# Optimization experiments

Measured on AMD Instinct MI355X. Metric: run time of the kernel, lower is better.

The kernel has to match this reference:

```python
import jax, jax.numpy as jnp
import numpy as np

N_JOINTS = 24

def _rodrigues(r):
    # r: [B, J, 3] axis-angle -> [B, J, 3, 3] rotation matrices
    theta = jnp.clip(jnp.linalg.norm(r, axis=-1, keepdims=True), 1e-6)  # [B,J,1]
    rh = r / theta
    z = jnp.zeros_like(rh[..., :1])
    # skew-symmetric matrix m
    m = jnp.stack([
        jnp.concatenate([z, -rh[..., 2:3], rh[..., 1:2]], -1),
        jnp.concatenate([rh[..., 2:3], z, -rh[..., 0:1]], -1),
        jnp.concatenate([-rh[..., 1:2], rh[..., 0:1], z], -1),
    ], axis=-2)  # [B,J,3,3]
    rrT = rh[..., :, None] * rh[..., None, :]  # outer product [B,J,3,3]
    cos = jnp.cos(theta)[..., None]
    sin = jnp.sin(theta)[..., None]
    eye = jnp.eye(3, dtype=r.dtype)
    return cos * eye + (1.0 - cos) * rrT + sin * m

def _with_zeros(Rm, t):
    # Rm: [B,3,3], t: [B,3] -> [B,4,4] homogeneous transform
    B = Rm.shape[0]
    top = jnp.concatenate([Rm, t[:, :, None]], axis=-1)  # [B,3,4]
    bot = jnp.broadcast_to(jnp.array([0.0, 0.0, 0.0, 1.0], Rm.dtype), (B, 1, 4))
    return jnp.concatenate([top, bot], axis=1)

def _keypoints(v, idx):
    # v: [B,N,3], idx: [G,K] vertex-index groups -> [B,G,3] via (max+min)/2
    g = v[:, idx]  # [B,G,K,3] irregular gather
    return (g.max(axis=2) + g.min(axis=2)) * 0.5

def setup_inputs() -> dict:
    key = jax.random.key(0)
    ks = jax.random.split(key, 8)
    B, N, P, K = 64, 40000, 100, 128
    beta = jax.random.normal(ks[0], (B, P), jnp.float32)
    pose = jax.random.normal(ks[1], (B, N_JOINTS * 3), jnp.float32) * 0.3
    trans = jax.random.normal(ks[2], (B, 3), jnp.float32)
    shapedirs = jax.random.normal(ks[3], (P, 3 * N), jnp.float32) * 0.01
    v_template = jax.random.normal(ks[4], (N, 3), jnp.float32)
    w = jax.random.uniform(ks[5], (N, N_JOINTS), jnp.float32)
    weights = w / w.sum(axis=1, keepdims=True)  # LBS weights sum to 1
    reorder_index = jnp.arange(N_JOINTS, dtype=jnp.int64 if jax.config.jax_enable_x64 else jnp.int32)
    # kinematic tree: parent[i] < i (binary-tree shape stands in for the rabbit skeleton)
    parent = jnp.concatenate([jnp.zeros(1, jnp.int32), (jnp.arange(1, N_JOINTS, dtype=jnp.int32) - 1) // 2])
    joint_idx = jax.random.randint(ks[6], (N_JOINTS - 1, K), 0, N)
    add_idx = jax.random.randint(ks[7], (7, K), 0, N)
    return {"beta": beta, "pose": pose, "trans": trans, "shapedirs": shapedirs,
            "v_template": v_template, "weights": weights, "reorder_index": reorder_index,
            "parent": parent, "joint_idx": joint_idx, "add_idx": add_idx}

def reference(beta, pose, trans, shapedirs, v_template, weights,
              reorder_index, parent, joint_idx, add_idx):
    B = beta.shape[0]
    pose = pose.reshape(B, N_JOINTS, 3)[:, reorder_index]
    # blend shapes: v_shaped = beta @ shapedirs + template
    v_posed = (beta @ shapedirs + v_template.reshape(-1)).reshape(B, -1, 3)  # [B,N,3]
    # joints from vertex-group (max+min)/2, root is zero
    J = jnp.concatenate([jnp.zeros((B, 1, 3), beta.dtype), _keypoints(v_posed, joint_idx)], axis=1)  # [B,24,3]
    R = _rodrigues(pose)  # [B,24,3,3]
    # forward kinematics along the tree (fixed 24-joint loop)
    par = np.asarray(jax.device_get(parent))
    G = [_with_zeros(R[:, 0], J[:, 0])]
    for i in range(1, N_JOINTS):
        p = int(par[i])
        G_loc = _with_zeros(R[:, i], J[:, i] - J[:, p])
        G.append(jnp.matmul(G[p], G_loc))
    G = jnp.stack(G, axis=1)  # [B,24,4,4]
    # remove rest-pose joint locations (pack subtraction only touches last column)
    Jh = jnp.concatenate([J, jnp.zeros((B, N_JOINTS, 1), beta.dtype)], axis=-1)[..., None]  # [B,24,4,1]
    t_corr = jnp.matmul(G, Jh)  # [B,24,4,1]
    G1 = jnp.concatenate([G[..., :3], G[..., 3:4] - t_corr], axis=-1)
    # LBS skinning: per-vertex blended transform
    T = jnp.einsum('nk,bkij->bnij', weights, G1)  # [B,N,4,4]
    vh = jnp.concatenate([v_posed, jnp.ones((B, v_posed.shape[1], 1), beta.dtype)], axis=-1)  # [B,N,4]
    posed = jnp.einsum('bnij,bnj->bni', T, vh)[..., :3] + trans[:, None, :]  # [B,N,3]
    skeleton = jnp.concatenate([
        jnp.zeros((B, 1, 3), beta.dtype),
        _keypoints(posed, joint_idx),
        _keypoints(posed, add_idx),
    ], axis=1)  # [B,31,3]
    return posed, skeleton
```

## Files before the change

### kernel.cpp

```cpp
#include <hip/hip_runtime.h>
#include <math.h>

#define B   64
#define NV  40000
#define P   100
#define KG  128
#define NJ  24
#define TV  16
#define NSK 31
#define NSUB (KG / TV)

typedef __attribute__((ext_vector_type(8))) short bf16x8;
typedef __attribute__((ext_vector_type(4))) float f32x4;

__device__ __forceinline__ unsigned short rne_bf16(float f) {
  unsigned u = __float_as_uint(f);
  u = (u + 0x7FFFu + ((u >> 16) & 1u)) >> 16;
  return (unsigned short)u;
}

__global__ __launch_bounds__(256)
void k_jpart(const float* __restrict__ beta,
             const float* __restrict__ sd,
             const float* __restrict__ vt,
             const int*   __restrict__ joint_idx,
             float*       __restrict__ pmn,
             float*       __restrict__ pmx) {
  const int j = blockIdx.x;
  const int s = blockIdx.y;
  const int t = threadIdx.x;
  const int lane = t & 63, wv = t >> 6;
  const int l15 = lane & 15, qd = lane >> 4;

  __shared__ __align__(16) unsigned short beta_s[64 * 136];
  __shared__ __align__(16) unsigned short sdT_s[48 * 136];
  __shared__ float vt_s[48];
  __shared__ int   idx_s[TV];
  float* pos_s = (float*)beta_s;

  if (t < TV) idx_s[t] = joint_idx[j * KG + s * TV + t];
  __syncthreads();

  for (int e = t; e < 64 * 36; e += 256) {
    const int m = e / 36, pp = P + e % 36;
    beta_s[m * 136 + pp] = 0;
  }
  for (int e = t; e < 64 * P; e += 256) {
    const int m = e / P, p = e % P;
    beta_s[m * 136 + p] = rne_bf16(beta[e]);
  }
  for (int task = t; task < 768; task += 256) {
    const int n = task % 48, kg = task / 48;
    const size_t colbase = (size_t)idx_s[n / 3] * 3 + (n % 3);
    unsigned pk[4];
#pragma unroll
    for (int h = 0; h < 4; ++h) {
      const int k0 = kg * 8 + 2 * h;
      float f0 = 0.0f, f1 = 0.0f;
      if (k0 < P)     f0 = sd[(size_t)k0 * (3 * NV) + colbase];
      if (k0 + 1 < P) f1 = sd[(size_t)(k0 + 1) * (3 * NV) + colbase];
      pk[h] = (unsigned)rne_bf16(f0) | ((unsigned)rne_bf16(f1) << 16);
    }
    *(uint4*)&sdT_s[n * 136 + kg * 8] = make_uint4(pk[0], pk[1], pk[2], pk[3]);
  }
  if (t < 48) vt_s[t] = vt[(size_t)idx_s[t / 3] * 3 + (t % 3)];
  __syncthreads();

  bf16x8 af[4];
#pragma unroll
  for (int ks = 0; ks < 4; ++ks)
    af[ks] = *(const bf16x8*)&beta_s[(wv * 16 + l15) * 136 + ks * 32 + qd * 8];
  f32x4 acc[3];
#pragma unroll
  for (int nt = 0; nt < 3; ++nt) acc[nt] = (f32x4){0.f, 0.f, 0.f, 0.f};
#pragma unroll
  for (int ks = 0; ks < 4; ++ks) {
#pragma unroll
    for (int nt = 0; nt < 3; ++nt) {
      const bf16x8 bf = *(const bf16x8*)&sdT_s[(nt * 16 + l15) * 136 + ks * 32 + qd * 8];
      acc[nt] = __builtin_amdgcn_mfma_f32_16x16x32_bf16(af[ks], bf, acc[nt], 0, 0, 0);
    }
  }
  float vtv[3];
#pragma unroll
  for (int nt = 0; nt < 3; ++nt) vtv[nt] = vt_s[nt * 16 + l15];
  __syncthreads();

#pragma unroll
  for (int nt = 0; nt < 3; ++nt) {
    const int n = nt * 16 + l15;
    const int v = n / 3, c = n - 3 * v;
#pragma unroll
    for (int r = 0; r < 4; ++r) {
      const int m = wv * 16 + qd * 4 + r;
      pos_s[m * 68 + v * 4 + c] = acc[nt][r] + vtv[nt];
    }
  }
  __syncthreads();

  if (t < 192) {
    const int b = t / 3, c = t % 3;
    float lo = 1e30f, hi = -1e30f;
#pragma unroll
    for (int v = 0; v < TV; ++v) {
      const float val = pos_s[b * 68 + v * 4 + c];
      lo = fminf(lo, val); hi = fmaxf(hi, val);
    }
    pmn[((j * NSUB + s) * B + b) * 3 + c] = lo;
    pmx[((j * NSUB + s) * B + b) * 3 + c] = hi;
  }
}

__global__ void k_chain(const float* __restrict__ pose,
                        const int*   __restrict__ parent,
                        const float* __restrict__ pmn,
                        const float* __restrict__ pmx,
                        const float* __restrict__ beta,
                        const float* __restrict__ trans,
                        unsigned short* __restrict__ G1A,
                        unsigned short* __restrict__ beta_bf) {
  const int b = blockIdx.x;
  const int t = threadIdx.x;

  __shared__ float R[NJ][9];
  __shared__ float Jl[NJ][3];
  __shared__ float G[NJ][12];
  __shared__ float G1c[NJ][12];

  if (t < NJ) {
    const float x = pose[b * NJ * 3 + t * 3 + 0];
    const float y = pose[b * NJ * 3 + t * 3 + 1];
    const float z = pose[b * NJ * 3 + t * 3 + 2];
    const float th = fmaxf(sqrtf(x * x + y * y + z * z), 1e-6f);
    const float xh = x / th, yh = y / th, zh = z / th;
    const float c = cosf(th), s = sinf(th), o = 1.0f - c;
    R[t][0] = c + o * xh * xh;      R[t][1] = o * xh * yh - s * zh; R[t][2] = o * xh * zh + s * yh;
    R[t][3] = o * xh * yh + s * zh; R[t][4] = c + o * yh * yh;      R[t][5] = o * yh * zh - s * xh;
    R[t][6] = o * xh * zh - s * yh; R[t][7] = o * yh * zh + s * xh; R[t][8] = c + o * zh * zh;
    if (t == 0) {
      Jl[0][0] = 0.0f; Jl[0][1] = 0.0f; Jl[0][2] = 0.0f;
    } else {
      const int jj = t - 1;
#pragma unroll
      for (int c2 = 0; c2 < 3; ++c2) {
        float lo = 1e30f, hi = -1e30f;
#pragma unroll
        for (int s2 = 0; s2 < NSUB; ++s2) {
          lo = fminf(lo, pmn[((jj * NSUB + s2) * B + b) * 3 + c2]);
          hi = fmaxf(hi, pmx[((jj * NSUB + s2) * B + b) * 3 + c2]);
        }
        Jl[t][c2] = 0.5f * (lo + hi);
      }
    }
  }
  __syncthreads();

  if (t < 12) {
    const int r = t >> 2, c = t & 3;
    G[0][t] = (c < 3) ? R[0][r * 3 + c] : Jl[0][r];
  }
  __syncthreads();

  for (int i = 1; i < NJ; ++i) {
    const int p = parent[i];
    if (t < 12) {
      const int r = t >> 2, c = t & 3;
      const float g0 = G[p][r * 4 + 0];
      const float g1 = G[p][r * 4 + 1];
      const float g2 = G[p][r * 4 + 2];
      float l0, l1, l2, add;
      if (c < 3) {
        l0 = R[i][0 * 3 + c]; l1 = R[i][1 * 3 + c]; l2 = R[i][2 * 3 + c];
        add = 0.0f;
      } else {
        l0 = Jl[i][0] - Jl[p][0]; l1 = Jl[i][1] - Jl[p][1]; l2 = Jl[i][2] - Jl[p][2];
        add = G[p][r * 4 + 3];
      }
      G[i][t] = g0 * l0 + g1 * l1 + g2 * l2 + add;
    }
    __syncthreads();
  }

  for (int e = t; e < NJ * 12; e += 64) {
    const int i = e / 12, rc = e % 12, r = rc >> 2, c = rc & 3;
    float val;
    if (c < 3) {
      val = G[i][rc];
    } else {
      val = G[i][r * 4 + 3] - (G[i][r * 4 + 0] * Jl[i][0] +
                               G[i][r * 4 + 1] * Jl[i][1] +
                               G[i][r * 4 + 2] * Jl[i][2]);
    }
    G1c[i][rc] = val;
  }
  __syncthreads();

  for (int e = t; e < 136; e += 64)
    beta_bf[b * 136 + e] = (e < P) ? rne_bf16(beta[b * P + e]) : (unsigned short)0;

  for (int e = t; e < 512; e += 64) {
    const int m = e >> 5, k = e & 31;
    float val = 0.0f;
    if (m < 12) {
      if (k < NJ) val = G1c[k][m];
      else if (k == NJ && (m & 3) == 3) val = trans[b * 3 + (m >> 2)];
    }
    G1A[(size_t)b * 512 + e] = rne_bf16(val);
  }
}

__global__ __launch_bounds__(256)
void k_skin(const float* __restrict__ sd,
            const float* __restrict__ vt,
            const float* __restrict__ w,
            const unsigned short* __restrict__ beta_bf,
            const unsigned short* __restrict__ G1A,
            float*       __restrict__ out) {
  const int n0v = blockIdx.x * TV;
  const int col0 = n0v * 3;
  const int t  = threadIdx.x;
  const int lane = t & 63, wv = t >> 6;
  const int l15 = lane & 15, q = lane >> 4;

  __shared__ __align__(16) unsigned short beta_s[64 * 136];
  __shared__ __align__(16) unsigned short sdT_s[48 * 136];
  __shared__ __align__(16) unsigned short wT_s[16 * 40];
  __shared__ float vt_s[48];
  float* vhf  = (float*)beta_s;
  float* pos_s = (float*)sdT_s;

  for (int e = t; e < 64 * 136 / 8; e += 256)
    ((uint4*)beta_s)[e] = ((const uint4*)beta_bf)[e];
  for (int task = t; task < 768; task += 256) {
    const int n = task % 48, kg = task / 48;
    unsigned pk[4];
#pragma unroll
    for (int h = 0; h < 4; ++h) {
      const int k0 = kg * 8 + 2 * h;
      float f0 = 0.0f, f1 = 0.0f;
      if (k0 < P)     f0 = sd[(size_t)k0 * (3 * NV) + col0 + n];
      if (k0 + 1 < P) f1 = sd[(size_t)(k0 + 1) * (3 * NV) + col0 + n];
      pk[h] = (unsigned)rne_bf16(f0) | ((unsigned)rne_bf16(f1) << 16);
    }
    *(uint4*)&sdT_s[n * 136 + kg * 8] = make_uint4(pk[0], pk[1], pk[2], pk[3]);
  }
  for (int e = t; e < 512; e += 256) {
    const int n = e >> 5, k = e & 31;
    float val = (k < NJ) ? w[(n0v + n) * NJ + k] : (k == NJ ? 1.0f : 0.0f);
    wT_s[n * 40 + k] = rne_bf16(val);
  }
  if (t < 48) vt_s[t] = vt[col0 + t];
  __syncthreads();

  bf16x8 af[4];
#pragma unroll
  for (int ks = 0; ks < 4; ++ks)
    af[ks] = *(const bf16x8*)&beta_s[(wv * 16 + l15) * 136 + ks * 32 + q * 8];
  f32x4 acc[3];
#pragma unroll
  for (int nt = 0; nt < 3; ++nt) acc[nt] = (f32x4){0.f, 0.f, 0.f, 0.f};
#pragma unroll
  for (int ks = 0; ks < 4; ++ks) {
#pragma unroll
    for (int nt = 0; nt < 3; ++nt) {
      const bf16x8 bf = *(const bf16x8*)&sdT_s[(nt * 16 + l15) * 136 + ks * 32 + q * 8];
      acc[nt] = __builtin_amdgcn_mfma_f32_16x16x32_bf16(af[ks], bf, acc[nt], 0, 0, 0);
    }
  }
  float vtv[3];
#pragma unroll
  for (int nt = 0; nt < 3; ++nt) vtv[nt] = vt_s[nt * 16 + l15];
  __syncthreads();

#pragma unroll
  for (int nt = 0; nt < 3; ++nt) {
    const int n = nt * 16 + l15;
    const int v = n / 3, c = n - 3 * v;
#pragma unroll
    for (int r = 0; r < 4; ++r) {
      const int m = wv * 16 + q * 4 + r;
      vhf[m * 68 + v * 4 + c] = acc[nt][r] + vtv[nt];
    }
  }
  __syncthreads();

  const bf16x8 wf = *(const bf16x8*)&wT_s[l15 * 40 + q * 8];
  const f32x4 zero = (f32x4){0.f, 0.f, 0.f, 0.f};
#pragma unroll 4
  for (int bi = 0; bi < 16; ++bi) {
    const int b = wv * 16 + bi;
    const bf16x8 gf = *(const bf16x8*)&G1A[(size_t)b * 512 + l15 * 32 + q * 8];
    const f32x4 d = __builtin_amdgcn_mfma_f32_16x16x32_bf16(gf, wf, zero, 0, 0, 0);
    const float4 vh = *(const float4*)&vhf[b * 68 + l15 * 4];
    if (q < 3) {
      const float pos = d[0] * vh.x + d[1] * vh.y + d[2] * vh.z + d[3];
      pos_s[b * 48 + l15 * 3 + q] = pos;
    }
  }
  __syncthreads();

  for (int e = t; e < 768; e += 256) {
    const int b = e / 12, ch = e % 12;
    const float4 val = *(const float4*)&pos_s[b * 48 + ch * 4];
    *(float4*)&out[(size_t)b * (NV * 3) + col0 + ch * 4] = val;
  }
}

__global__ void k_skel(const float* __restrict__ posed,
                       const int*   __restrict__ joint_idx,
                       const int*   __restrict__ add_idx,
                       float*       __restrict__ skel) {
  const int j = blockIdx.x;
  const int b = blockIdx.y;
  const int t = threadIdx.x;
  const int idx = (j < 23) ? joint_idx[j * KG + t] : add_idx[(j - 23) * KG + t];

  const float* p = posed + (size_t)b * NV * 3 + (size_t)idx * 3;
  float mn[3], mx[3];
#pragma unroll
  for (int c = 0; c < 3; ++c) { mn[c] = p[c]; mx[c] = p[c]; }
#pragma unroll
  for (int off = 32; off > 0; off >>= 1) {
#pragma unroll
    for (int c = 0; c < 3; ++c) {
      mn[c] = fminf(mn[c], __shfl_down(mn[c], off));
      mx[c] = fmaxf(mx[c], __shfl_down(mx[c], off));
    }
  }
  __shared__ float s_mn[2][3], s_mx[2][3];
  const int wave = t >> 6, lane = t & 63;
  if (lane == 0) {
#pragma unroll
    for (int c = 0; c < 3; ++c) { s_mn[wave][c] = mn[c]; s_mx[wave][c] = mx[c]; }
  }
  __syncthreads();
  if (t == 0) {
#pragma unroll
    for (int c = 0; c < 3; ++c) {
      float lo = fminf(s_mn[0][c], s_mn[1][c]);
      float hi = fmaxf(s_mx[0][c], s_mx[1][c]);
      skel[(b * NSK + 1 + j) * 3 + c] = 0.5f * (lo + hi);
      if (j == 0) skel[(b * NSK + 0) * 3 + c] = 0.0f;
    }
  }
}

extern "C" void kernel_launch(void* const* d_in, const int* in_sizes, int n_in,
                              void* d_out, int out_size, void* d_ws, size_t ws_size,
                              hipStream_t stream) {
  const float* beta     = (const float*)d_in[0];
  const float* pose     = (const float*)d_in[1];
  const float* trans    = (const float*)d_in[2];
  const float* sd       = (const float*)d_in[3];
  const float* vt       = (const float*)d_in[4];
  const float* w        = (const float*)d_in[5];
  const int* parent     = (const int*)d_in[7];
  const int* joint_idx  = (const int*)d_in[8];
  const int* add_idx    = (const int*)d_in[9];

  float* out = (float*)d_out;
  unsigned short* G1A     = (unsigned short*)d_ws;
  unsigned short* beta_bf = G1A + B * 512;
  float* pmn = (float*)(beta_bf + B * 136);
  float* pmx = pmn + 23 * NSUB * B * 3;

  k_jpart<<<dim3(23, NSUB), 256, 0, stream>>>(beta, sd, vt, joint_idx, pmn, pmx);
  k_chain<<<B, 64, 0, stream>>>(pose, parent, pmn, pmx, beta, trans, G1A, beta_bf);
  k_skin <<<NV / TV, 256, 0, stream>>>(sd, vt, w, beta_bf, G1A, out);
  k_skel <<<dim3(30, B), 128, 0, stream>>>(out, joint_idx, add_idx,
                                           out + (size_t)B * NV * 3);
}
```

Baseline: 156.6 us.

## Stream shapedirs, beta, weights straight into MFMA registers, dropping LDS staging

A small prep kernel now converts beta to bf16 once. k_jpart and k_skin read the bf16 beta fragments straight from global memory instead of staging them in LDS. k_skin also loads shapedirs, the template vertices and the skinning weights directly into MFMA operand registers, and writes posed vertices straight to global without the LDS transpose and float4 store. This removes LDS traffic and barriers and lowers shared memory per block to allow more occupancy, at the cost of scattered global stores and repeated, less coalesced global reads of beta per wave.

New measurement: 158.4 us. No clear change (+1.1%).

```diff
diff --git a/kernel.cpp b/kernel.cpp
--- a/kernel.cpp
+++ b/kernel.cpp
@@ -19,8 +19,17 @@
   return (unsigned short)u;
 }
 
+__global__ void k_prep(const float* __restrict__ beta,
+                       unsigned short* __restrict__ beta_bf) {
+  const int t = blockIdx.x * 256 + threadIdx.x;
+  if (t < B * 136) {
+    const int m = t / 136, k = t % 136;
+    beta_bf[t] = (k < P) ? rne_bf16(beta[m * P + k]) : (unsigned short)0;
+  }
+}
+
 __global__ __launch_bounds__(256)
-void k_jpart(const float* __restrict__ beta,
+void k_jpart(const unsigned short* __restrict__ beta_bf,
              const float* __restrict__ sd,
              const float* __restrict__ vt,
              const int*   __restrict__ joint_idx,
@@ -32,23 +41,14 @@
   const int lane = t & 63, wv = t >> 6;
   const int l15 = lane & 15, qd = lane >> 4;
 
-  __shared__ __align__(16) unsigned short beta_s[64 * 136];
   __shared__ __align__(16) unsigned short sdT_s[48 * 136];
+  __shared__ __align__(16) float pos_s[64 * 68];
   __shared__ float vt_s[48];
   __shared__ int   idx_s[TV];
-  float* pos_s = (float*)beta_s;
 
   if (t < TV) idx_s[t] = joint_idx[j * KG + s * TV + t];
   __syncthreads();
 
-  for (int e = t; e < 64 * 36; e += 256) {
-    const int m = e / 36, pp = P + e % 36;
-    beta_s[m * 136 + pp] = 0;
-  }
-  for (int e = t; e < 64 * P; e += 256) {
-    const int m = e / P, p = e % P;
-    beta_s[m * 136 + p] = rne_bf16(beta[e]);
-  }
   for (int task = t; task < 768; task += 256) {
     const int n = task % 48, kg = task / 48;
     const size_t colbase = (size_t)idx_s[n / 3] * 3 + (n % 3);
@@ -66,25 +66,21 @@
   if (t < 48) vt_s[t] = vt[(size_t)idx_s[t / 3] * 3 + (t % 3)];
   __syncthreads();
 
-  bf16x8 af[4];
-#pragma unroll
-  for (int ks = 0; ks < 4; ++ks)
-    af[ks] = *(const bf16x8*)&beta_s[(wv * 16 + l15) * 136 + ks * 32 + qd * 8];
   f32x4 acc[3];
 #pragma unroll
   for (int nt = 0; nt < 3; ++nt) acc[nt] = (f32x4){0.f, 0.f, 0.f, 0.f};
 #pragma unroll
   for (int ks = 0; ks < 4; ++ks) {
+    const bf16x8 af = *(const bf16x8*)&beta_bf[(wv * 16 + l15) * 136 + ks * 32 + qd * 8];
 #pragma unroll
     for (int nt = 0; nt < 3; ++nt) {
       const bf16x8 bf = *(const bf16x8*)&sdT_s[(nt * 16 + l15) * 136 + ks * 32 + qd * 8];
-      acc[nt] = __builtin_amdgcn_mfma_f32_16x16x32_bf16(af[ks], bf, acc[nt], 0, 0, 0);
+      acc[nt] = __builtin_amdgcn_mfma_f32_16x16x32_bf16(af, bf, acc[nt], 0, 0, 0);
     }
   }
   float vtv[3];
 #pragma unroll
   for (int nt = 0; nt < 3; ++nt) vtv[nt] = vt_s[nt * 16 + l15];
-  __syncthreads();
 
 #pragma unroll
   for (int nt = 0; nt < 3; ++nt) {
@@ -115,10 +111,8 @@
                         const int*   __restrict__ parent,
                         const float* __restrict__ pmn,
                         const float* __restrict__ pmx,
-                        const float* __restrict__ beta,
                         const float* __restrict__ trans,
-                        unsigned short* __restrict__ G1A,
-                        unsigned short* __restrict__ beta_bf) {
+                        unsigned short* __restrict__ G1A) {
   const int b = blockIdx.x;
   const int t = threadIdx.x;
 
@@ -195,9 +189,6 @@
   }
   __syncthreads();
 
-  for (int e = t; e < 136; e += 64)
-    beta_bf[b * 136 + e] = (e < P) ? rne_bf16(beta[b * P + e]) : (unsigned short)0;
-
   for (int e = t; e < 512; e += 64) {
     const int m = e >> 5, k = e & 31;
     float val = 0.0f;
@@ -222,55 +213,35 @@
   const int lane = t & 63, wv = t >> 6;
   const int l15 = lane & 15, q = lane >> 4;
 
-  __shared__ __align__(16) unsigned short beta_s[64 * 136];
-  __shared__ __align__(16) unsigned short sdT_s[48 * 136];
-  __shared__ __align__(16) unsigned short wT_s[16 * 40];
-  __shared__ float vt_s[48];
-  float* vhf  = (float*)beta_s;
-  float* pos_s = (float*)sdT_s;
-
-  for (int e = t; e < 64 * 136 / 8; e += 256)
-    ((uint4*)beta_s)[e] = ((const uint4*)beta_bf)[e];
-  for (int task = t; task < 768; task += 256) {
-    const int n = task % 48, kg = task / 48;
-    unsigned pk[4];
-#pragma unroll
-    for (int h = 0; h < 4; ++h) {
-      const int k0 = kg * 8 + 2 * h;
-      float f0 = 0.0f, f1 = 0.0f;
-      if (k0 < P)     f0 = sd[(size_t)k0 * (3 * NV) + col0 + n];
-      if (k0 + 1 < P) f1 = sd[(size_t)(k0 + 1) * (3 * NV) + col0 + n];
-      pk[h] = (unsigned)rne_bf16(f0) | ((unsigned)rne_bf16(f1) << 16);
-    }
-    *(uint4*)&sdT_s[n * 136 + kg * 8] = make_uint4(pk[0], pk[1], pk[2], pk[3]);
-  }
-  for (int e = t; e < 512; e += 256) {
-    const int n = e >> 5, k = e & 31;
-    float val = (k < NJ) ? w[(n0v + n) * NJ + k] : (k == NJ ? 1.0f : 0.0f);
-    wT_s[n * 40 + k] = rne_bf16(val);
-  }
-  if (t < 48) vt_s[t] = vt[col0 + t];
-  __syncthreads();
-
-  bf16x8 af[4];
-#pragma unroll
-  for (int ks = 0; ks < 4; ++ks)
-    af[ks] = *(const bf16x8*)&beta_s[(wv * 16 + l15) * 136 + ks * 32 + q * 8];
+  __shared__ __align__(16) float vhf[64 * 68];
+
   f32x4 acc[3];
 #pragma unroll
   for (int nt = 0; nt < 3; ++nt) acc[nt] = (f32x4){0.f, 0.f, 0.f, 0.f};
 #pragma unroll
   for (int ks = 0; ks < 4; ++ks) {
+    const bf16x8 af = *(const bf16x8*)&beta_bf[(wv * 16 + l15) * 136 + ks * 32 + q * 8];
 #pragma unroll
     for (int nt = 0; nt < 3; ++nt) {
-      const bf16x8 bf = *(const bf16x8*)&sdT_s[(nt * 16 + l15) * 136 + ks * 32 + q * 8];
-      acc[nt] = __builtin_amdgcn_mfma_f32_16x16x32_bf16(af[ks], bf, acc[nt], 0, 0, 0);
+      float bv[8];
+#pragma unroll
+      for (int jj = 0; jj < 8; ++jj) {
+        const int k = ks * 32 + q * 8 + jj;
+        if (ks < 3) {
+          bv[jj] = sd[(size_t)k * (3 * NV) + col0 + nt * 16 + l15];
+        } else {
+          bv[jj] = (k < P) ? sd[(size_t)k * (3 * NV) + col0 + nt * 16 + l15] : 0.0f;
+        }
+      }
+      bf16x8 bfr;
+#pragma unroll
+      for (int jj = 0; jj < 8; ++jj) bfr[jj] = (short)rne_bf16(bv[jj]);
+      acc[nt] = __builtin_amdgcn_mfma_f32_16x16x32_bf16(af, bfr, acc[nt], 0, 0, 0);
     }
   }
   float vtv[3];
 #pragma unroll
-  for (int nt = 0; nt < 3; ++nt) vtv[nt] = vt_s[nt * 16 + l15];
-  __syncthreads();
+  for (int nt = 0; nt < 3; ++nt) vtv[nt] = vt[col0 + nt * 16 + l15];
 
 #pragma unroll
   for (int nt = 0; nt < 3; ++nt) {
@@ -284,7 +255,19 @@
   }
   __syncthreads();
 
-  const bf16x8 wf = *(const bf16x8*)&wT_s[l15 * 40 + q * 8];
+  bf16x8 wf;
+  if (q < 3) {
+    const float* wrow = &w[(size_t)(n0v + l15) * NJ + q * 8];
+    const float4 w0 = *(const float4*)wrow;
+    const float4 w1 = *(const float4*)(wrow + 4);
+    wf[0] = (short)rne_bf16(w0.x); wf[1] = (short)rne_bf16(w0.y);
+    wf[2] = (short)rne_bf16(w0.z); wf[3] = (short)rne_bf16(w0.w);
+    wf[4] = (short)rne_bf16(w1.x); wf[5] = (short)rne_bf16(w1.y);
+    wf[6] = (short)rne_bf16(w1.z); wf[7] = (short)rne_bf16(w1.w);
+  } else {
+    wf = (bf16x8){0, 0, 0, 0, 0, 0, 0, 0};
+    wf[0] = (short)0x3F80;
+  }
   const f32x4 zero = (f32x4){0.f, 0.f, 0.f, 0.f};
 #pragma unroll 4
   for (int bi = 0; bi < 16; ++bi) {
@@ -293,16 +276,9 @@
     const f32x4 d = __builtin_amdgcn_mfma_f32_16x16x32_bf16(gf, wf, zero, 0, 0, 0);
     const float4 vh = *(const float4*)&vhf[b * 68 + l15 * 4];
     if (q < 3) {
-      const float pos = d[0] * vh.x + d[1] * vh.y + d[2] * vh.z + d[3];
-      pos_s[b * 48 + l15 * 3 + q] = pos;
-    }
-  }
-  __syncthreads();
-
-  for (int e = t; e < 768; e += 256) {
-    const int b = e / 12, ch = e % 12;
-    const float4 val = *(const float4*)&pos_s[b * 48 + ch * 4];
-    *(float4*)&out[(size_t)b * (NV * 3) + col0 + ch * 4] = val;
+      out[(size_t)b * (NV * 3) + col0 + l15 * 3 + q] =
+          d[0] * vh.x + d[1] * vh.y + d[2] * vh.z + d[3];
+    }
   }
 }
 
@@ -364,8 +340,9 @@
   float* pmn = (float*)(beta_bf + B * 136);
   float* pmx = pmn + 23 * NSUB * B * 3;
 
-  k_jpart<<<dim3(23, NSUB), 256, 0, stream>>>(beta, sd, vt, joint_idx, pmn, pmx);
-  k_chain<<<B, 64, 0, stream>>>(pose, parent, pmn, pmx, beta, trans, G1A, beta_bf);
+  k_prep <<<(B * 136 + 255) / 256, 256, 0, stream>>>(beta, beta_bf);
+  k_jpart<<<dim3(23, NSUB), 256, 0, stream>>>(beta_bf, sd, vt, joint_idx, pmn, pmx);
+  k_chain<<<B, 64, 0, stream>>>(pose, parent, pmn, pmx, trans, G1A);
   k_skin <<<NV / TV, 256, 0, stream>>>(sd, vt, w, beta_bf, G1A, out);
   k_skel <<<dim3(30, B), 128, 0, stream>>>(out, joint_idx, add_idx,
                                            out + (size_t)B * NV * 3);
```
